# Kernel optimization log

Hardware: AMD Instinct MI355X
Metric: run time of the kernel (lower is better)

## Reference

```python
import jax, jax.numpy as jnp
import numpy as np


def _silu(x):
    return x * jax.nn.sigmoid(x)


def _ln(x, w, b, eps=1e-5):
    mu = x.mean(-1, keepdims=True)
    xc = x - mu
    var = (xc * xc).mean(-1, keepdims=True)
    return xc * jax.lax.rsqrt(var + eps) * w + b


def _segsum(a):
    # a: (..., Q) -> (..., Q, Q) lower-triangular cumulative segment sums
    Q = a.shape[-1]
    cs = jnp.cumsum(a, axis=-1)
    ss = cs[..., :, None] - cs[..., None, :]
    mask = jnp.tril(jnp.ones((Q, Q), dtype=bool))
    return jnp.where(mask, ss, -jnp.inf)


def _ssd(x, A, Bm, Cm, chunk=64):
    # Mamba2 SSD dual (chunked) form. x:(b,l,h,p) pre-scaled by dt, A:(b,l,h)=dt*A, Bm/Cm:(b,l,n)
    b, l, h, p = x.shape
    c = l // chunk
    x = x.reshape(b, c, chunk, h, p)
    A = A.reshape(b, c, chunk, h).transpose(0, 3, 1, 2)          # (b,h,c,q)
    Bm = Bm.reshape(b, c, chunk, -1)
    Cm = Cm.reshape(b, c, chunk, -1)
    Acs = jnp.cumsum(A, axis=-1)                                  # (b,h,c,q)
    Lmat = jnp.exp(_segsum(A))                                    # (b,h,c,q,q)
    Yd = jnp.einsum('bcln,bcsn,bhcls,bcshp->bclhp', Cm, Bm, Lmat, x)
    dec = jnp.exp(Acs[..., -1:] - Acs)                            # (b,h,c,q)
    states = jnp.einsum('bcln,bhcl,bclhp->bchpn', Bm, dec, x)     # (b,c,h,p,n)
    cdec = jnp.exp(Acs[..., -1]).transpose(2, 0, 1)               # (c,b,h)
    st = states.transpose(1, 0, 2, 3, 4)                          # (c,b,h,p,n)

    def step(carry, inp):
        s, d = inp
        return carry * d[..., None, None] + s, carry

    _, prev = jax.lax.scan(step, jnp.zeros_like(st[0]), (st, cdec))
    prev = prev.transpose(1, 0, 2, 3, 4)                          # (b,c,h,p,n)
    Yo = jnp.einsum('bcln,bchpn,bhcl->bclhp', Cm, prev, jnp.exp(Acs))
    return (Yd + Yo).reshape(b, l, h, p)


def _mamba(x, in_w, in_b, conv_w, conv_b, A_log, D, dt_bias, rms_w, out_w, headdim, d_state):
    b, l, _ = x.shape
    nh = A_log.shape[0]
    di = nh * headdim
    zxbcdt = x @ in_w.T + in_b
    z = zxbcdt[..., :di]
    xBC = zxbcdt[..., di:2 * di + 2 * d_state]
    dt = jax.nn.softplus(zxbcdt[..., -nh:] + dt_bias)             # (b,l,nh)
    K = conv_w.shape[-1]
    xp = jnp.pad(xBC, ((0, 0), (K - 1, 0), (0, 0)))               # causal depthwise conv
    xBC = sum(xp[:, k:k + l, :] * conv_w[:, k] for k in range(K))
    xBC = _silu(xBC + conv_b)
    xs = xBC[..., :di].reshape(b, l, nh, headdim)
    Bm = xBC[..., di:di + d_state]
    Cm = xBC[..., di + d_state:]
    A = -jnp.exp(A_log)
    y = _ssd(xs * dt[..., None], dt * A, Bm, Cm)
    y = y + D[None, None, :, None] * xs
    y = y.reshape(b, l, di) * _silu(z)                            # gated RMSNorm
    y = y * jax.lax.rsqrt(jnp.mean(y * y, -1, keepdims=True) + 1e-5) * rms_w
    return y @ out_w.T


def setup_inputs() -> dict:
    key = jax.random.key(0)
    ks = iter(jax.random.split(key, 64))

    def nrm(shape, s):
        return jax.random.normal(next(ks), shape, jnp.float32) * s

    d = {}
    d['x'] = jax.random.normal(next(ks), (4, 128, 64, 64), jnp.float32)
    d['seed_tok_w'] = nrm((8, 128), 0.08)
    d['seed_tok_b'] = jnp.zeros((8,), jnp.float32)
    d['seed_detok_w'] = nrm((128, 8), 0.3)
    d['seed_detok_b'] = jnp.zeros((128,), jnp.float32)
    d['sm_in_w'] = nrm((66, 8), 0.3)
    d['sm_in_b'] = jnp.zeros((66,), jnp.float32)
    d['sm_conv_w'] = nrm((48, 3), 0.3)
    d['sm_conv_b'] = jnp.zeros((48,), jnp.float32)
    d['sm_A_log'] = jnp.log(jnp.arange(1, 3, dtype=jnp.float32))
    d['sm_D'] = jnp.ones((2,), jnp.float32)
    d['sm_dt_bias'] = jnp.full((2,), -4.0, jnp.float32)
    d['sm_rms_w'] = jnp.ones((16,), jnp.float32)
    d['sm_out_w'] = nrm((8, 16), 0.2)
    d['cm_in_w'] = nrm((2, 196, 16), 0.2)
    d['cm_in_b'] = jnp.zeros((2, 196), jnp.float32)
    d['cm_conv_w'] = nrm((2, 160, 3), 0.3)
    d['cm_conv_b'] = jnp.zeros((2, 160), jnp.float32)
    d['cm_A_log'] = jnp.tile(jnp.log(jnp.arange(1, 5, dtype=jnp.float32)), (2, 1))
    d['cm_D'] = jnp.ones((2, 4), jnp.float32)
    d['cm_dt_bias'] = jnp.full((2, 4), -4.0, jnp.float32)
    d['cm_rms_w'] = jnp.ones((2, 32), jnp.float32)
    d['cm_out_w'] = nrm((2, 16, 32), 0.15)
    d['cross_W'] = jnp.eye(8, dtype=jnp.float32) + 0.01 * jax.random.normal(next(ks), (8, 8), jnp.float32)
    d['norm1_w'] = jnp.ones((128,), jnp.float32)
    d['norm1_b'] = jnp.zeros((128,), jnp.float32)
    d['norm2_w'] = jnp.ones((128,), jnp.float32)
    d['norm2_b'] = jnp.zeros((128,), jnp.float32)
    d['fc1_w'] = nrm((256, 128), 0.08)
    d['fc1_b'] = jnp.zeros((256,), jnp.float32)
    d['dw_w'] = nrm((256, 1, 3, 3), 0.2)
    d['dw_b'] = jnp.zeros((256,), jnp.float32)
    d['fc2_w'] = nrm((128, 256), 0.06)
    d['fc2_b'] = jnp.zeros((128,), jnp.float32)
    d['skip_scale'] = jnp.ones((1,), jnp.float32)
    return d


def reference(x, seed_tok_w, seed_tok_b, seed_detok_w, seed_detok_b,
              sm_in_w, sm_in_b, sm_conv_w, sm_conv_b, sm_A_log, sm_D, sm_dt_bias, sm_rms_w, sm_out_w,
              cm_in_w, cm_in_b, cm_conv_w, cm_conv_b, cm_A_log, cm_D, cm_dt_bias, cm_rms_w, cm_out_w,
              cross_W, norm1_w, norm1_b, norm2_w, norm2_b,
              fc1_w, fc1_b, dw_w, dw_b, fc2_w, fc2_b, skip_scale):
    B, C, H, W = x.shape
    L = H * W
    # --- GlobalSeed ---
    g = jnp.einsum('bchw,gc->bghw', x, seed_tok_w) + seed_tok_b[None, :, None, None]
    gf = g.reshape(B, -1, L).transpose(0, 2, 1)                   # (B,L,G)
    gf = _mamba(gf, sm_in_w, sm_in_b, sm_conv_w, sm_conv_b, sm_A_log, sm_D,
                sm_dt_bias, sm_rms_w, sm_out_w, 8, 16) + gf
    det = jnp.einsum('blg,cg->blc', gf, seed_detok_w) + seed_detok_b
    seed = x + det.transpose(0, 2, 1).reshape(B, C, H, W)
    # --- split-channel cascaded SSD (shared weights across splits) ---
    xn = _ln(x.reshape(B, C, L).transpose(0, 2, 1), norm1_w, norm1_b)   # (B,L,C)
    S = cross_W.shape[0]
    xs = jnp.stack(jnp.split(xn, S, axis=-1))                     # (S,B,L,C/S)

    def cascade(xi):
        for i in range(cm_in_w.shape[0]):
            xi = _mamba(xi, cm_in_w[i], cm_in_b[i], cm_conv_w[i], cm_conv_b[i],
                        cm_A_log[i], cm_D[i], cm_dt_bias[i], cm_rms_w[i], cm_out_w[i], 8, 64)
        return xi

    ys = jax.vmap(cascade)(xs) + xs * skip_scale
    # --- SubCrossToken mixing ---
    gm = ys.mean(axis=2)                                          # (S,B,Cs)
    wsm = jax.nn.softmax(cross_W, axis=1)
    gmix = jnp.einsum('qbc,qp->pbc', gm, wsm)
    ys = ys + gmix[:, :, None, :]
    out = ys.transpose(1, 2, 0, 3).reshape(B, L, -1)
    out = _ln(out, norm2_w, norm2_b)
    out = out.transpose(0, 2, 1).reshape(B, C, H, W) + seed
    # --- ConvFFN ---
    h1 = jnp.einsum('bchw,oc->bohw', out, fc1_w) + fc1_b[None, :, None, None]
    dw = jax.lax.conv_general_dilated(h1, dw_w, (1, 1), 'SAME',
                                      feature_group_count=h1.shape[1],
                                      dimension_numbers=('NCHW', 'OIHW', 'NCHW'))
    h2 = jax.nn.gelu(dw + dw_b[None, :, None, None])
    ffn = jnp.einsum('bohw,co->bchw', h2, fc2_w) + fc2_b[None, :, None, None]
    return out + ffn
```

## Files before the change

### kernel.cpp

```cpp
#include <hip/hip_runtime.h>
#include <math.h>

#define B_ 4
#define CCH 128
#define HH 64
#define WW 64
#define LL 4096
#define NCHK 64

__device__ __forceinline__ float siluf(float x) { return x / (1.f + __expf(-x)); }
__device__ __forceinline__ float softplusf(float x) { return (x > 20.f) ? x : log1pf(__expf(x)); }
__device__ __forceinline__ int swz(int n, int l) {
  return (n << 6) + ((((l >> 2) ^ ((n >> 2) & 15)) << 2) | (l & 3));
}

__global__ __launch_bounds__(256) void k_seedtok(const float* __restrict__ x,
    const float* __restrict__ w, const float* __restrict__ bias, float* __restrict__ gf)
{
  __shared__ float sw[8*128];
  int tid = threadIdx.x;
  for (int i = tid; i < 1024; i += 256) sw[i] = w[i];
  __syncthreads();
  int idx = blockIdx.x * 256 + tid;
  int b = idx / LL, l = idx % LL;
  const float* xp = x + (size_t)b*CCH*LL + l;
  float acc[8];
#pragma unroll
  for (int g = 0; g < 8; ++g) acc[g] = bias[g];
  for (int c = 0; c < CCH; ++c) {
    float xv = xp[(size_t)c*LL];
#pragma unroll
    for (int g = 0; g < 8; ++g) acc[g] += xv * sw[g*128 + c];
  }
  float* o = gf + (size_t)idx*8;
#pragma unroll
  for (int g = 0; g < 8; ++g) o[g] = acc[g];
}

template<int DIN, int NZ, int NDS, int NDT>
__global__ __launch_bounds__(256) void k_inproj(
    const float* __restrict__ src, int srcMode,
    const float* __restrict__ in_w, const float* __restrict__ in_b,
    const float* __restrict__ conv_w, const float* __restrict__ conv_b,
    const float* __restrict__ dt_bias,
    float* __restrict__ zb, float* __restrict__ dtb,
    float* __restrict__ xsb, float* __restrict__ Bb, float* __restrict__ Cb)
{
  constexpr int NXBC = NZ + 2*NDS;
  constexpr int NTOT = 2*NZ + 2*NDS + NDT;
  constexpr int NZQ  = NZ/4;
  constexpr int NDSQ = NDS/4;
  constexpr int XP   = DIN + 1;
  __shared__ float xt[66*XP];
  __shared__ float wl[NTOT*DIN];
  __shared__ float cwl[NXBC*3];
  __shared__ float cbl[NXBC];
  __shared__ float ibl[NTOT];
  __shared__ float dts[64*NDT];
  __shared__ float hp[NXBC*2];
  int tid = threadIdx.x;
  int seq = blockIdx.x >> 6;
  int l0  = (blockIdx.x & 63) << 6;
  for (int i = tid; i < NTOT*DIN; i += 256) wl[i] = in_w[i];
  for (int i = tid; i < NXBC*3; i += 256) cwl[i] = conv_w[i];
  for (int i = tid; i < NXBC; i += 256) cbl[i] = conv_b[i];
  for (int i = tid; i < NTOT; i += 256) ibl[i] = in_b[i];
  const float* sp; int sstr;
  if (srcMode == 0) { sp = src + (size_t)seq*LL*DIN; sstr = DIN; }
  else { sp = src + (size_t)(seq & 3)*LL*CCH + (seq >> 2)*16; sstr = CCH; }
  for (int i = tid; i < 66*DIN; i += 256) {
    int r = i / DIN, d = i % DIN;
    int l = l0 - 2 + r;
    xt[r*XP + d] = (l >= 0) ? sp[(size_t)l*sstr + d] : 0.f;
  }
  __syncthreads();
  for (int i = tid; i < 2*NXBC; i += 256) {
    int t = i & 1, ch = i >> 1;
    const float* wr = &wl[(NZ + ch)*DIN];
    const float* xp = &xt[t*XP];
    float acc = 0.f;
#pragma unroll
    for (int d = 0; d < DIN; ++d) acc += xp[d]*wr[d];
    hp[ch*2 + t] = acc;
  }
  __syncthreads();
  int l = tid & 63, w4 = tid >> 6;
  float xr2[DIN];
#pragma unroll
  for (int d = 0; d < DIN; ++d) xr2[d] = xt[(l+2)*XP + d];
  size_t gl = (size_t)seq*LL + l0 + l;
  int tok = l0 + l;
  float v0ok = (tok >= 2) ? 1.f : 0.f;
  float v1ok = (tok >= 1) ? 1.f : 0.f;
  {
    float zv[NZQ];
#pragma unroll
    for (int j = 0; j < NZQ; ++j) {
      int row = w4*NZQ + j;
      const float* wr = &wl[row*DIN];
      float acc = ibl[row];
#pragma unroll
      for (int d = 0; d < DIN; ++d) acc += xr2[d]*wr[d];
      zv[j] = acc;
    }
#pragma unroll
    for (int g = 0; g < NZQ/4; ++g)
      *(float4*)&zb[gl*NZ + w4*NZQ + 4*g] = make_float4(zv[4*g], zv[4*g+1], zv[4*g+2], zv[4*g+3]);
  }
  if (w4 < NDT) {
    int row = NTOT - NDT + w4;
    const float* wr = &wl[row*DIN];
    float acc = ibl[row] + dt_bias[w4];
#pragma unroll
    for (int d = 0; d < DIN; ++d) acc += xr2[d]*wr[d];
    dts[l*NDT + w4] = softplusf(acc);
  }
  auto convch = [&](int ch) -> float {
    int row = NZ + ch;
    const float* wr = &wl[row*DIN];
    float pm = 0.f;
#pragma unroll
    for (int d = 0; d < DIN; ++d) pm += xr2[d]*wr[d];
    float m1 = __shfl_up(pm, 1, 64);
    float m2 = __shfl_up(pm, 2, 64);
    float h0 = hp[ch*2 + 0], h1 = hp[ch*2 + 1];
    if (l == 0) m1 = h1;
    m2 = (l == 0) ? h0 : ((l == 1) ? h1 : m2);
    float ib = ibl[row];
    float conv = cbl[ch] + (m2+ib)*v0ok*cwl[ch*3+0] + (m1+ib)*v1ok*cwl[ch*3+1] + (pm+ib)*cwl[ch*3+2];
    return siluf(conv);
  };
  {
    float xv[NZQ];
#pragma unroll
    for (int j = 0; j < NZQ; ++j) xv[j] = convch(w4*NZQ + j);
#pragma unroll
    for (int g = 0; g < NZQ/4; ++g)
      *(float4*)&xsb[gl*NZ + w4*NZQ + 4*g] = make_float4(xv[4*g], xv[4*g+1], xv[4*g+2], xv[4*g+3]);
  }
  {
    float bv[NDSQ];
#pragma unroll
    for (int j = 0; j < NDSQ; ++j) bv[j] = convch(NZ + w4*NDSQ + j);
#pragma unroll
    for (int g = 0; g < NDSQ/4; ++g)
      *(float4*)&Bb[gl*NDS + w4*NDSQ + 4*g] = make_float4(bv[4*g], bv[4*g+1], bv[4*g+2], bv[4*g+3]);
  }
  {
    float cv[NDSQ];
#pragma unroll
    for (int j = 0; j < NDSQ; ++j) cv[j] = convch(NZ + NDS + w4*NDSQ + j);
#pragma unroll
    for (int g = 0; g < NDSQ/4; ++g)
      *(float4*)&Cb[gl*NDS + w4*NDSQ + 4*g] = make_float4(cv[4*g], cv[4*g+1], cv[4*g+2], cv[4*g+3]);
  }
  __syncthreads();
  if (tid < 64) {
    if constexpr (NDT == 4) {
      *(float4*)&dtb[((size_t)seq*LL + l0 + tid)*4] =
          make_float4(dts[tid*4], dts[tid*4+1], dts[tid*4+2], dts[tid*4+3]);
    } else {
      *(float2*)&dtb[((size_t)seq*LL + l0 + tid)*NDT] = make_float2(dts[tid*NDT], dts[tid*NDT+1]);
    }
  }
}

template<int DS, int NH>
__global__ __launch_bounds__(256) void k_ssd1(
    const float* __restrict__ xs, const float* __restrict__ dtb,
    const float* __restrict__ Bb, const float* __restrict__ Cb,
    const float* __restrict__ A_log,
    float* __restrict__ ybuf, float* __restrict__ states,
    float* __restrict__ cdec, float* __restrict__ acsOut)
{
  constexpr int DI = NH*8;
  constexpr int NG = DS/4;
  __shared__ __align__(16) float BtBl[DS*64];
  __shared__ __align__(16) float CtGt[64*64];
  __shared__ __align__(16) float xde[NH*64*8];
  int tid = threadIdx.x;
  int cid = blockIdx.x & 63;
  int seq = blockIdx.x >> 6;
  int l0  = cid << 6;
  for (int i = tid; i < 16*DS; i += 256) {
    int ng = i % NG, l = i / NG;
    size_t g = ((size_t)seq*LL + l0 + l)*DS + 4*ng;
    float4 bv = *(const float4*)&Bb[g];
    float4 cv = *(const float4*)&Cb[g];
    BtBl[swz(4*ng+0, l)] = bv.x; BtBl[swz(4*ng+1, l)] = bv.y;
    BtBl[swz(4*ng+2, l)] = bv.z; BtBl[swz(4*ng+3, l)] = bv.w;
    CtGt[swz(4*ng+0, l)] = cv.x; CtGt[swz(4*ng+1, l)] = cv.y;
    CtGt[swz(4*ng+2, l)] = cv.z; CtGt[swz(4*ng+3, l)] = cv.w;
  }
  __syncthreads();
  int lt = (tid >> 4) << 2, st = (tid & 15) << 2;
  float acc[4][4] = {};
#pragma unroll 4
  for (int n = 0; n < DS; ++n) {
    float4 cv = *(const float4*)&CtGt[swz(n, lt)];
    float4 bv = *(const float4*)&BtBl[swz(n, st)];
    float cc[4] = {cv.x, cv.y, cv.z, cv.w};
    float bb[4] = {bv.x, bv.y, bv.z, bv.w};
#pragma unroll
    for (int i2 = 0; i2 < 4; ++i2)
#pragma unroll
      for (int j2 = 0; j2 < 4; ++j2)
        acc[i2][j2] += cc[i2]*bb[j2];
  }
  __syncthreads();
#pragma unroll
  for (int j = 0; j < 4; ++j) {
    float4 gv = make_float4(acc[0][j], acc[1][j], acc[2][j], acc[3][j]);
    *(float4*)&CtGt[swz(st + j, lt)] = gv;
  }
  for (int i = tid; i < 16*DS; i += 256) {
    int ng = i % NG, l = i / NG;
    float4 bv = *(const float4*)&Bb[((size_t)seq*LL + l0 + l)*DS + 4*ng];
    *(float4*)&BtBl[l*DS + 4*ng] = bv;
  }
  __syncthreads();
  int w = tid >> 6, lane = tid & 63;
  if (w < NH) {
    int h = w;
    float dt_l = dtb[((size_t)seq*LL + l0 + lane)*NH + h];
    float Aval = -__expf(A_log[h]);
    float v = dt_l * Aval;
#pragma unroll
    for (int off = 1; off < 64; off <<= 1) {
      float t = __shfl_up(v, off, 64);
      if (lane >= off) v += t;
    }
    float acs_l = v;
    float m = __shfl(v, 31, 64);
    float acsLast = __shfl(v, 63, 64);
    float el = __expf(fminf(acs_l - m, 60.f));
    float fl = __expf(fminf(m - acs_l, 60.f));
    const float* xp = &xs[((size_t)seq*LL + l0 + lane)*DI + h*8];
    float4 x0 = *(const float4*)xp, x1 = *(const float4*)(xp + 4);
    float s1 = dt_l*fl;
    float* xe = &xde[(h*64 + lane)*8];
    *(float4*)xe     = make_float4(x0.x*s1, x0.y*s1, x0.z*s1, x0.w*s1);
    *(float4*)(xe+4) = make_float4(x1.x*s1, x1.y*s1, x1.z*s1, x1.w*s1);
    int lg = lane >> 2, lm = lane & 3;
    float ya[8] = {0,0,0,0,0,0,0,0};
#pragma unroll 4
    for (int s = 0; s < 64; ++s) {
      float g = CtGt[(s << 6) + ((((lg ^ ((s >> 2) & 15))) << 2) | lm)];
      g = (s <= lane) ? g : 0.f;
      const float* xr = &xde[(h*64 + s)*8];
      float4 a0 = *(const float4*)xr, a1 = *(const float4*)(xr + 4);
      ya[0] += g*a0.x; ya[1] += g*a0.y; ya[2] += g*a0.z; ya[3] += g*a0.w;
      ya[4] += g*a1.x; ya[5] += g*a1.y; ya[6] += g*a1.z; ya[7] += g*a1.w;
    }
    float* yp = &ybuf[((size_t)seq*LL + l0 + lane)*DI + h*8];
    *(float4*)yp     = make_float4(ya[0]*el, ya[1]*el, ya[2]*el, ya[3]*el);
    *(float4*)(yp+4) = make_float4(ya[4]*el, ya[5]*el, ya[6]*el, ya[7]*el);
    if (lane < DS) {
      float r2 = __expf(acsLast - m);
      float sa[8] = {0,0,0,0,0,0,0,0};
#pragma unroll 4
      for (int ll = 0; ll < 64; ++ll) {
        float b = BtBl[ll*DS + lane];
        const float* xr = &xde[(h*64 + ll)*8];
        float4 a0 = *(const float4*)xr, a1 = *(const float4*)(xr + 4);
        sa[0] += b*a0.x; sa[1] += b*a0.y; sa[2] += b*a0.z; sa[3] += b*a0.w;
        sa[4] += b*a1.x; sa[5] += b*a1.y; sa[6] += b*a1.z; sa[7] += b*a1.w;
      }
      float* sp2 = &states[(((size_t)seq*NH + h)*NCHK + cid)*(size_t)(8*DS) + lane*8];
      *(float4*)sp2     = make_float4(sa[0]*r2, sa[1]*r2, sa[2]*r2, sa[3]*r2);
      *(float4*)(sp2+4) = make_float4(sa[4]*r2, sa[5]*r2, sa[6]*r2, sa[7]*r2);
    }
    if (lane == 63) cdec[((size_t)seq*NH + h)*NCHK + cid] = __expf(acsLast);
    acsOut[((size_t)seq*NH + h)*LL + l0 + lane] = acs_l;
  }
}

__global__ __launch_bounds__(512) void k_scan(float* __restrict__ st, const float* __restrict__ cd, int PN)
{
  int tid = threadIdx.x;
  size_t base = (size_t)blockIdx.x * NCHK * PN + tid;
  const float* c = cd + (size_t)blockIdx.x * NCHK;
  float carry = 0.f;
  for (int k = 0; k < NCHK; ++k) {
    size_t a = base + (size_t)k*PN;
    float s = st[a];
    st[a] = carry;
    carry = carry*c[k] + s;
  }
}

template<int DS, int NH>
__global__ __launch_bounds__(256) void k_ssd_yo(
    float* __restrict__ ybuf, const float* __restrict__ Cb,
    const float* __restrict__ prevSt, const float* __restrict__ acsG,
    const float* __restrict__ Dp, const float* __restrict__ xs)
{
  constexpr int DI = NH*8;
  constexpr int NG = DS/4;
  __shared__ __align__(16) float Ct2[DS*64];
  __shared__ __align__(16) float pvs[NH*DS*8];
  int tid = threadIdx.x;
  int cid = blockIdx.x & 63;
  int seq = blockIdx.x >> 6;
  int l0  = cid << 6;
  for (int i = tid; i < 16*DS; i += 256) {
    int ng = i % NG, l = i / NG;
    float4 cv = *(const float4*)&Cb[((size_t)seq*LL + l0 + l)*DS + 4*ng];
    Ct2[swz(4*ng+0, l)] = cv.x; Ct2[swz(4*ng+1, l)] = cv.y;
    Ct2[swz(4*ng+2, l)] = cv.z; Ct2[swz(4*ng+3, l)] = cv.w;
  }
  for (int i = tid; i < NH*DS*8; i += 256) {
    int h = i / (DS*8), r = i % (DS*8);
    pvs[i] = prevSt[(((size_t)seq*NH + h)*NCHK + cid)*(size_t)(DS*8) + r];
  }
  __syncthreads();
  int w = tid >> 6, lane = tid & 63;
  if (w < NH) {
    int h = w;
    float el = __expf(acsG[((size_t)seq*NH + h)*LL + l0 + lane]);
    float Dh = Dp[h];
    int lg = lane >> 2, lm = lane & 3;
    float acc[8] = {0,0,0,0,0,0,0,0};
#pragma unroll 4
    for (int n = 0; n < DS; ++n) {
      float c = Ct2[(n << 6) + ((((lg ^ ((n >> 2) & 15))) << 2) | lm)];
      const float* pr = &pvs[(h*DS + n)*8];
      float4 p0 = *(const float4*)pr, p1 = *(const float4*)(pr + 4);
      acc[0] += c*p0.x; acc[1] += c*p0.y; acc[2] += c*p0.z; acc[3] += c*p0.w;
      acc[4] += c*p1.x; acc[5] += c*p1.y; acc[6] += c*p1.z; acc[7] += c*p1.w;
    }
    size_t gi = ((size_t)seq*LL + l0 + lane)*DI + h*8;
    float4 y0 = *(const float4*)&ybuf[gi], y1 = *(const float4*)&ybuf[gi+4];
    float4 xv0 = *(const float4*)&xs[gi], xv1 = *(const float4*)&xs[gi+4];
    y0.x += el*acc[0] + Dh*xv0.x; y0.y += el*acc[1] + Dh*xv0.y;
    y0.z += el*acc[2] + Dh*xv0.z; y0.w += el*acc[3] + Dh*xv0.w;
    y1.x += el*acc[4] + Dh*xv1.x; y1.y += el*acc[5] + Dh*xv1.y;
    y1.z += el*acc[6] + Dh*xv1.z; y1.w += el*acc[7] + Dh*xv1.w;
    *(float4*)&ybuf[gi] = y0; *(float4*)&ybuf[gi+4] = y1;
  }
}

template<int DI, int DOUT>
__global__ __launch_bounds__(256) void k_gate(
    const float* __restrict__ ybuf, const float* __restrict__ zbuf,
    const float* __restrict__ rms_w, const float* __restrict__ out_w,
    float* __restrict__ dst, int resMode, const float* __restrict__ res,
    const float* __restrict__ skipPtr)
{
  __shared__ float ow[DOUT*DI];
  __shared__ float rw[DI];
  int tid = threadIdx.x;
  for (int i = tid; i < DOUT*DI; i += 256) ow[i] = out_w[i];
  for (int i = tid; i < DI; i += 256) rw[i] = rms_w[i];
  __syncthreads();
  size_t idx = (size_t)blockIdx.x*256 + tid;
  float y[DI];
  const float* yp = ybuf + idx*DI;
  const float* zp = zbuf + idx*DI;
  float ss = 0.f;
#pragma unroll
  for (int i = 0; i < DI; ++i) {
    float z = zp[i];
    float g = yp[i] * (z / (1.f + __expf(-z)));
    y[i] = g; ss += g*g;
  }
  float r = rsqrtf(ss*(1.f/DI) + 1e-5f);
#pragma unroll
  for (int i = 0; i < DI; ++i) y[i] *= r*rw[i];
  const float* rp = nullptr; float skip = 1.f;
  int seq = (int)(idx / LL), l = (int)(idx % LL);
  if (resMode == 1) rp = res + idx*DOUT;
  else if (resMode == 2) {
    int s = seq / B_, b = seq % B_;
    rp = res + ((size_t)b*LL + l)*CCH + s*DOUT;
    skip = skipPtr[0];
  }
  float* dp = dst + idx*DOUT;
#pragma unroll
  for (int o = 0; o < DOUT; ++o) {
    float acc = 0.f;
#pragma unroll
    for (int i = 0; i < DI; ++i) acc += y[i]*ow[o*DI + i];
    if (rp) acc += skip * rp[o];
    dp[o] = acc;
  }
}

__global__ __launch_bounds__(256) void k_ln1(const float* __restrict__ x,
    const float* __restrict__ w, const float* __restrict__ bb, float* __restrict__ xn)
{
  __shared__ float tile[128*65];
  __shared__ float mu[64], rs[64];
  int tid = threadIdx.x;
  int b = blockIdx.x >> 6;
  int l0 = (blockIdx.x & 63) << 6;
  for (int i = tid; i < 8192; i += 256) {
    int l = i & 63, c = i >> 6;
    tile[c*65 + l] = x[((size_t)b*CCH + c)*LL + l0 + l];
  }
  __syncthreads();
  if (tid < 64) {
    float s = 0.f;
    for (int c = 0; c < CCH; ++c) s += tile[c*65 + tid];
    float m = s * (1.f/CCH);
    float v = 0.f;
    for (int c = 0; c < CCH; ++c) { float d = tile[c*65 + tid] - m; v += d*d; }
    mu[tid] = m; rs[tid] = rsqrtf(v*(1.f/CCH) + 1e-5f);
  }
  __syncthreads();
  for (int i = tid; i < 8192; i += 256) {
    int c = i & 127, l = i >> 7;
    xn[((size_t)b*LL + l0 + l)*CCH + c] = (tile[c*65 + l] - mu[l])*rs[l]*w[c] + bb[c];
  }
}

__global__ __launch_bounds__(256) void k_gm(const float* __restrict__ ys, float* __restrict__ gm)
{
  __shared__ float red[256];
  int tid = threadIdx.x;
  int seq = blockIdx.x;
  int c = tid & 15, lane = tid >> 4;
  float s = 0.f;
  for (int l = lane; l < LL; l += 16) s += ys[((size_t)seq*LL + l)*16 + c];
  red[tid] = s;
  __syncthreads();
  if (tid < 16) {
    float t = 0.f;
    for (int g = 0; g < 16; ++g) t += red[g*16 + tid];
    gm[(size_t)seq*16 + tid] = t * (1.f/LL);
  }
}

__global__ __launch_bounds__(256) void k_mix(const float* __restrict__ gm,
    const float* __restrict__ crossW, float* __restrict__ gmix)
{
  __shared__ float wsm[64];
  int tid = threadIdx.x;
  if (tid < 8) {
    float mx = -1e30f;
    for (int p = 0; p < 8; ++p) mx = fmaxf(mx, crossW[tid*8 + p]);
    float e[8]; float s = 0.f;
    for (int p = 0; p < 8; ++p) { e[p] = __expf(crossW[tid*8 + p] - mx); s += e[p]; }
    for (int p = 0; p < 8; ++p) wsm[tid*8 + p] = e[p] / s;
  }
  __syncthreads();
  for (int i = tid; i < 512; i += 256) {
    int c = i & 15; int bb = (i >> 4) & 3; int p = i >> 6;
    float acc = 0.f;
    for (int q = 0; q < 8; ++q) acc += gm[((size_t)(q*B_ + bb))*16 + c] * wsm[q*8 + p];
    gmix[((size_t)(p*B_ + bb))*16 + c] = acc;
  }
}

__global__ __launch_bounds__(256) void k_out2(const float* __restrict__ ys,
    const float* __restrict__ gmix, const float* __restrict__ w, const float* __restrict__ bb,
    const float* __restrict__ x, const float* __restrict__ gf2,
    const float* __restrict__ dw, const float* __restrict__ db,
    float* __restrict__ outb)
{
  __shared__ float tile[128*65];
  __shared__ float mu[64], rs[64];
  int tid = threadIdx.x;
  int b = blockIdx.x >> 6;
  int l0 = (blockIdx.x & 63) << 6;
  for (int i = tid; i < 8192; i += 256) {
    int c = i & 15; int l = (i >> 4) & 63; int s = i >> 10;
    int seq = s*B_ + b;
    tile[(s*16 + c)*65 + l] = ys[((size_t)seq*LL + l0 + l)*16 + c] + gmix[(size_t)seq*16 + c];
  }
  __syncthreads();
  if (tid < 64) {
    float sm = 0.f;
    for (int c = 0; c < 128; ++c) sm += tile[c*65 + tid];
    float m = sm * (1.f/128.f);
    float v = 0.f;
    for (int c = 0; c < 128; ++c) { float d = tile[c*65 + tid] - m; v += d*d; }
    mu[tid] = m; rs[tid] = rsqrtf(v*(1.f/128.f) + 1e-5f);
  }
  __syncthreads();
  int lfix = tid & 63;
  float g8[8];
  {
    const float* gp = gf2 + ((size_t)b*LL + l0 + lfix)*8;
#pragma unroll
    for (int k = 0; k < 8; ++k) g8[k] = gp[k];
  }
  for (int i = tid; i < 8192; i += 256) {
    int l = i & 63, c = i >> 6;
    size_t gi = ((size_t)b*CCH + c)*LL + l0 + l;
    float det = db[c];
#pragma unroll
    for (int k = 0; k < 8; ++k) det += g8[k]*dw[c*8 + k];
    outb[gi] = (tile[c*65 + l] - mu[l])*rs[l]*w[c] + bb[c] + x[gi] + det;
  }
}

__global__ __launch_bounds__(256) void k_fc1(const float* __restrict__ src,
    const float* __restrict__ w, const float* __restrict__ bias, float* __restrict__ dst)
{
  constexpr int WP = 129;
  __shared__ float st[128*64];
  __shared__ float wt[64*WP];
  int tid = threadIdx.x;
  int blk = blockIdx.x;
  int ot = blk & 3;
  int lt = (blk >> 2) & 63;
  int b  = blk >> 8;
  int l0 = lt << 6, o0 = ot << 6;
  for (int i = tid; i < 8192; i += 256) {
    int l = i & 63, c = i >> 6;
    st[c*64 + l] = src[((size_t)b*CCH + c)*LL + l0 + l];
  }
  for (int i = tid; i < 8192; i += 256) {
    int c = i & 127, o = i >> 7;
    wt[o*WP + c] = w[(size_t)(o0 + o)*128 + c];
  }
  __syncthreads();
  int l4 = (tid & 15) << 2, o4 = (tid >> 4) << 2;
  float a0[4] = {}, a1[4] = {}, a2[4] = {}, a3[4] = {};
#pragma unroll 4
  for (int c = 0; c < 128; ++c) {
    float4 sv = *(float4*)&st[c*64 + l4];
    float w0 = wt[(o4+0)*WP + c];
    float w1 = wt[(o4+1)*WP + c];
    float w2 = wt[(o4+2)*WP + c];
    float w3 = wt[(o4+3)*WP + c];
    a0[0] += w0*sv.x; a0[1] += w0*sv.y; a0[2] += w0*sv.z; a0[3] += w0*sv.w;
    a1[0] += w1*sv.x; a1[1] += w1*sv.y; a1[2] += w1*sv.z; a1[3] += w1*sv.w;
    a2[0] += w2*sv.x; a2[1] += w2*sv.y; a2[2] += w2*sv.z; a2[3] += w2*sv.w;
    a3[0] += w3*sv.x; a3[1] += w3*sv.y; a3[2] += w3*sv.z; a3[3] += w3*sv.w;
  }
  float* rows[4] = {a0, a1, a2, a3};
#pragma unroll
  for (int j = 0; j < 4; ++j) {
    int o = o0 + o4 + j;
    float bi = bias[o];
    float* a = rows[j];
    *(float4*)&dst[((size_t)b*256 + o)*LL + l0 + l4] =
        make_float4(a[0]+bi, a[1]+bi, a[2]+bi, a[3]+bi);
  }
}

__global__ __launch_bounds__(256) void k_dw(const float* __restrict__ h1,
    const float* __restrict__ w, const float* __restrict__ bias, float* __restrict__ h2)
{
  __shared__ float tile[66*66];
  int tid = threadIdx.x;
  int blk = blockIdx.x;
  const float* base = h1 + (size_t)blk*LL;
  const float* wp = w + (blk & 255)*9;
  float bi = bias[blk & 255];
  for (int i = tid; i < 66*66; i += 256) {
    int r = i / 66, cc = i % 66;
    int gr = r - 1, gc = cc - 1;
    tile[i] = (gr >= 0 && gr < HH && gc >= 0 && gc < WW) ? base[gr*WW + gc] : 0.f;
  }
  float w00 = wp[0], w01 = wp[1], w02 = wp[2];
  float w10 = wp[3], w11 = wp[4], w12 = wp[5];
  float w20 = wp[6], w21 = wp[7], w22 = wp[8];
  __syncthreads();
  float* outp = h2 + (size_t)blk*LL;
#pragma unroll
  for (int k = 0; k < 16; ++k) {
    int j = tid + k*256;
    int row = j >> 6, col = j & 63;
    const float* t0 = &tile[row*66 + col];
    float acc = t0[0]*w00  + t0[1]*w01  + t0[2]*w02
              + t0[66]*w10 + t0[67]*w11 + t0[68]*w12
              + t0[132]*w20 + t0[133]*w21 + t0[134]*w22;
    float v = acc + bi;
    float u = 0.7978845608028654f*(v + 0.044715f*v*v*v);
    float e = __expf(2.f*u);
    float th = 1.f - 2.f/(e + 1.f);
    outp[j] = 0.5f*v*(1.f + th);
  }
}

__global__ __launch_bounds__(256) void k_fc2(const float* __restrict__ h2,
    const float* __restrict__ w, const float* __restrict__ bias,
    const float* __restrict__ resid, float* __restrict__ dst)
{
  constexpr int WP = 260;
  __shared__ float st[128*64];
  __shared__ float wt[32*WP];
  int tid = threadIdx.x;
  int blk = blockIdx.x;
  int ct = blk & 3;
  int lt = (blk >> 2) & 63;
  int b  = blk >> 8;
  int l0 = lt << 6, c0 = ct << 5;
  for (int i = tid; i < 32*256; i += 256) {
    int o = i & 255, c = i >> 8;
    wt[c*WP + o] = w[(size_t)(c0 + c)*256 + o];
  }
  int l4 = (tid & 15) << 2, c2 = (tid >> 4) << 1;
  float a0[4] = {}, a1[4] = {};
  for (int ko = 0; ko < 256; ko += 128) {
    __syncthreads();
    for (int i = tid; i < 8192; i += 256) {
      int l = i & 63, o = i >> 6;
      st[o*64 + l] = h2[((size_t)b*256 + ko + o)*LL + l0 + l];
    }
    __syncthreads();
#pragma unroll 4
    for (int o = 0; o < 128; ++o) {
      float4 sv = *(float4*)&st[o*64 + l4];
      float w0 = wt[(c2+0)*WP + ko + o];
      float w1 = wt[(c2+1)*WP + ko + o];
      a0[0] += w0*sv.x; a0[1] += w0*sv.y; a0[2] += w0*sv.z; a0[3] += w0*sv.w;
      a1[0] += w1*sv.x; a1[1] += w1*sv.y; a1[2] += w1*sv.z; a1[3] += w1*sv.w;
    }
  }
  float* rows[2] = {a0, a1};
#pragma unroll
  for (int j = 0; j < 2; ++j) {
    int c = c0 + c2 + j;
    float bi = bias[c];
    size_t gi = ((size_t)b*CCH + c)*LL + l0 + l4;
    float4 rv = *(const float4*)&resid[gi];
    float* a = rows[j];
    *(float4*)&dst[gi] = make_float4(a[0]+bi+rv.x, a[1]+bi+rv.y, a[2]+bi+rv.z, a[3]+bi+rv.w);
  }
}

extern "C" void kernel_launch(void* const* d_in, const int* in_sizes, int n_in,
                              void* d_out, int out_size, void* d_ws, size_t ws_size,
                              hipStream_t stream) {
  (void)in_sizes; (void)n_in; (void)out_size; (void)ws_size;
  const float* x        = (const float*)d_in[0];
  const float* tok_w    = (const float*)d_in[1];
  const float* tok_b    = (const float*)d_in[2];
  const float* detok_w  = (const float*)d_in[3];
  const float* detok_b  = (const float*)d_in[4];
  const float* sm_in_w  = (const float*)d_in[5];
  const float* sm_in_b  = (const float*)d_in[6];
  const float* sm_conv_w= (const float*)d_in[7];
  const float* sm_conv_b= (const float*)d_in[8];
  const float* sm_A_log = (const float*)d_in[9];
  const float* sm_D     = (const float*)d_in[10];
  const float* sm_dt_b  = (const float*)d_in[11];
  const float* sm_rms_w = (const float*)d_in[12];
  const float* sm_out_w = (const float*)d_in[13];
  const float* cm_in_w  = (const float*)d_in[14];
  const float* cm_in_b  = (const float*)d_in[15];
  const float* cm_conv_w= (const float*)d_in[16];
  const float* cm_conv_b= (const float*)d_in[17];
  const float* cm_A_log = (const float*)d_in[18];
  const float* cm_D     = (const float*)d_in[19];
  const float* cm_dt_b  = (const float*)d_in[20];
  const float* cm_rms_w = (const float*)d_in[21];
  const float* cm_out_w = (const float*)d_in[22];
  const float* cross_W  = (const float*)d_in[23];
  const float* n1w      = (const float*)d_in[24];
  const float* n1b      = (const float*)d_in[25];
  const float* n2w      = (const float*)d_in[26];
  const float* n2b      = (const float*)d_in[27];
  const float* fc1w     = (const float*)d_in[28];
  const float* fc1b     = (const float*)d_in[29];
  const float* dww      = (const float*)d_in[30];
  const float* dwb      = (const float*)d_in[31];
  const float* fc2w     = (const float*)d_in[32];
  const float* fc2b     = (const float*)d_in[33];
  const float* skp      = (const float*)d_in[34];
  float* ws  = (float*)d_ws;
  float* out = (float*)d_out;

  const size_t SGF0 = 0;
  const size_t SOUTn= 131072;
  const size_t XN   = 2097152;
  const size_t YS   = 4194304;
  const size_t OUTB = 6291456;
  const size_t GM   = 8388608;
  const size_t GMIX = 8389120;
  const size_t SCR  = 8389632;
  const size_t CZ   = SCR;
  const size_t CDT  = CZ   + 4194304;
  const size_t CXS  = CDT  + 524288;
  const size_t CBF  = CXS  + 4194304;
  const size_t CCF  = CBF  + 8388608;
  const size_t CACS = CCF  + 8388608;
  const size_t CST  = CACS + 2097152;
  const size_t CCD  = CST  + 4194304;
  const size_t CY   = CCD  + 8192;
  const size_t XB   = CY   + 4194304;
  const size_t SZ   = SCR;
  const size_t SDT  = SZ  + 262144;
  const size_t SXS  = SDT + 32768;
  const size_t SB   = SXS + 262144;
  const size_t SC   = SB  + 262144;
  const size_t SACS = SC  + 262144;
  const size_t SST  = SACS + 32768;
  const size_t SCD  = SST + 65536;
  const size_t SY   = SCD + 512;
  const size_t H1 = SCR;
  const size_t H2 = SCR + 4194304;

  k_seedtok<<<64, 256, 0, stream>>>(x, tok_w, tok_b, ws + SGF0);
  k_inproj<8,16,16,2><<<B_*64, 256, 0, stream>>>(ws + SGF0, 0, sm_in_w, sm_in_b, sm_conv_w,
      sm_conv_b, sm_dt_b, ws + SZ, ws + SDT, ws + SXS, ws + SB, ws + SC);
  k_ssd1<16,2><<<B_*NCHK, 256, 0, stream>>>(ws + SXS, ws + SDT, ws + SB, ws + SC,
      sm_A_log, ws + SY, ws + SST, ws + SCD, ws + SACS);
  k_scan<<<B_*2, 128, 0, stream>>>(ws + SST, ws + SCD, 128);
  k_ssd_yo<16,2><<<B_*NCHK, 256, 0, stream>>>(ws + SY, ws + SC, ws + SST, ws + SACS, sm_D, ws + SXS);
  k_gate<16,8><<<B_*LL/256, 256, 0, stream>>>(ws + SY, ws + SZ, sm_rms_w, sm_out_w,
      ws + SOUTn, 1, ws + SGF0, skp);

  k_ln1<<<B_*64, 256, 0, stream>>>(x, n1w, n1b, ws + XN);

  k_inproj<16,32,64,4><<<32*64, 256, 0, stream>>>(ws + XN, 1, cm_in_w, cm_in_b, cm_conv_w,
      cm_conv_b, cm_dt_b, ws + CZ, ws + CDT, ws + CXS, ws + CBF, ws + CCF);
  k_ssd1<64,4><<<32*NCHK, 256, 0, stream>>>(ws + CXS, ws + CDT, ws + CBF, ws + CCF,
      cm_A_log, ws + CY, ws + CST, ws + CCD, ws + CACS);
  k_scan<<<32*4, 512, 0, stream>>>(ws + CST, ws + CCD, 512);
  k_ssd_yo<64,4><<<32*NCHK, 256, 0, stream>>>(ws + CY, ws + CCF, ws + CST, ws + CACS, cm_D, ws + CXS);
  k_gate<32,16><<<32*LL/256, 256, 0, stream>>>(ws + CY, ws + CZ, cm_rms_w, cm_out_w,
      ws + XB, 0, nullptr, skp);

  k_inproj<16,32,64,4><<<32*64, 256, 0, stream>>>(ws + XB, 0, cm_in_w + 3136, cm_in_b + 196,
      cm_conv_w + 480, cm_conv_b + 160, cm_dt_b + 4, ws + CZ, ws + CDT, ws + CXS, ws + CBF, ws + CCF);
  k_ssd1<64,4><<<32*NCHK, 256, 0, stream>>>(ws + CXS, ws + CDT, ws + CBF, ws + CCF,
      cm_A_log + 4, ws + CY, ws + CST, ws + CCD, ws + CACS);
  k_scan<<<32*4, 512, 0, stream>>>(ws + CST, ws + CCD, 512);
  k_ssd_yo<64,4><<<32*NCHK, 256, 0, stream>>>(ws + CY, ws + CCF, ws + CST, ws + CACS, cm_D + 4, ws + CXS);
  k_gate<32,16><<<32*LL/256, 256, 0, stream>>>(ws + CY, ws + CZ, cm_rms_w + 32, cm_out_w + 512,
      ws + YS, 2, ws + XN, skp);

  k_gm<<<32, 256, 0, stream>>>(ws + YS, ws + GM);
  k_mix<<<1, 256, 0, stream>>>(ws + GM, cross_W, ws + GMIX);
  k_out2<<<B_*64, 256, 0, stream>>>(ws + YS, ws + GMIX, n2w, n2b,
      x, ws + SOUTn, detok_w, detok_b, ws + OUTB);

  k_fc1<<<B_*64*4, 256, 0, stream>>>(ws + OUTB, fc1w, fc1b, ws + H1);
  k_dw<<<B_*256, 256, 0, stream>>>(ws + H1, dww, dwb, ws + H2);
  k_fc2<<<B_*64*4, 256, 0, stream>>>(ws + H2, fc2w, fc2b, ws + OUTB, out);
}
```

Before: 647.1 us.

## Fuse in-projection, causal conv and SSD chunk kernel for cross-Mamba layers

Adds a k_inssd kernel that performs the input projection, the causal depthwise conv with SiLU, dt softplus, and the intra-chunk SSD (diagonal block and chunk states) in a single block per chunk. The B matrix and dt stay in shared memory and registers instead of going to global scratch, and the separate inproj and ssd1 launches for both cascade layers are replaced. Halo rows for the conv are recomputed through a small pre-pass. Shared memory use (~54KB) and the launch-bounds occupancy hint could limit occupancy relative to the two separate kernels.

```diff
diff --git a/kernel.cpp b/kernel.cpp
--- a/kernel.cpp
+++ b/kernel.cpp
@@ -163,6 +163,197 @@
       *(float2*)&dtb[((size_t)seq*LL + l0 + tid)*NDT] = make_float2(dts[tid*NDT], dts[tid*NDT+1]);
     }
   }
+}
+
+__global__ __launch_bounds__(256, 3) void k_inssd(
+    const float* __restrict__ src, int srcMode,
+    const float* __restrict__ in_w, const float* __restrict__ in_b,
+    const float* __restrict__ conv_w, const float* __restrict__ conv_b,
+    const float* __restrict__ dt_bias, const float* __restrict__ A_log,
+    float* __restrict__ zb, float* __restrict__ xsb, float* __restrict__ Cb,
+    float* __restrict__ ybuf, float* __restrict__ states,
+    float* __restrict__ cdec, float* __restrict__ acsOut)
+{
+  const int DIN = 16, NZ = 32, NDS = 64, DI = 32;
+  const int NXBC = 160, NTOT = 196, XP = 17;
+  __shared__ float sm[13606];
+  float* Bl  = sm;
+  float* Ct  = sm + 4096;
+  float* U   = sm + 8192;
+  float* xt  = U;
+  float* wl  = U + 1122;
+  float* cwl = U + 4258;
+  float* cbl = U + 4738;
+  float* ibl = U + 4898;
+  float* hp  = U + 5094;
+  float* xde = U;
+  int tid = threadIdx.x;
+  int cid = blockIdx.x & 63;
+  int seq = blockIdx.x >> 6;
+  int l0  = cid << 6;
+  for (int i = tid; i < NTOT*DIN; i += 256) wl[i] = in_w[i];
+  for (int i = tid; i < NXBC*3; i += 256) cwl[i] = conv_w[i];
+  for (int i = tid; i < NXBC; i += 256) cbl[i] = conv_b[i];
+  for (int i = tid; i < NTOT; i += 256) ibl[i] = in_b[i];
+  const float* sp; int sstr;
+  if (srcMode == 0) { sp = src + (size_t)seq*LL*DIN; sstr = DIN; }
+  else { sp = src + (size_t)(seq & 3)*LL*CCH + (seq >> 2)*16; sstr = CCH; }
+  for (int i = tid; i < 66*DIN; i += 256) {
+    int r = i / DIN, d = i % DIN;
+    int l = l0 - 2 + r;
+    xt[r*XP + d] = (l >= 0) ? sp[(size_t)l*sstr + d] : 0.f;
+  }
+  __syncthreads();
+  for (int i = tid; i < 2*NXBC; i += 256) {
+    int t = i & 1, ch = i >> 1;
+    const float* wr = &wl[(NZ + ch)*DIN];
+    const float* xp = &xt[t*XP];
+    float acc = 0.f;
+#pragma unroll
+    for (int d = 0; d < DIN; ++d) acc += xp[d]*wr[d];
+    hp[ch*2 + t] = acc;
+  }
+  __syncthreads();
+  int lane = tid & 63, w = tid >> 6;
+  float xr2[DIN];
+#pragma unroll
+  for (int d = 0; d < DIN; ++d) xr2[d] = xt[(lane+2)*XP + d];
+  size_t gl = (size_t)seq*LL + l0 + lane;
+  int tok = l0 + lane;
+  float v0ok = (tok >= 2) ? 1.f : 0.f;
+  float v1ok = (tok >= 1) ? 1.f : 0.f;
+  {
+    float zv[8];
+#pragma unroll
+    for (int j = 0; j < 8; ++j) {
+      int row = w*8 + j;
+      const float* wr = &wl[row*DIN];
+      float acc = ibl[row];
+#pragma unroll
+      for (int d = 0; d < DIN; ++d) acc += xr2[d]*wr[d];
+      zv[j] = acc;
+    }
+    *(float4*)&zb[gl*NZ + w*8 + 0] = make_float4(zv[0], zv[1], zv[2], zv[3]);
+    *(float4*)&zb[gl*NZ + w*8 + 4] = make_float4(zv[4], zv[5], zv[6], zv[7]);
+  }
+  float dtv;
+  {
+    int row = NTOT - 4 + w;
+    const float* wr = &wl[row*DIN];
+    float acc = ibl[row] + dt_bias[w];
+#pragma unroll
+    for (int d = 0; d < DIN; ++d) acc += xr2[d]*wr[d];
+    dtv = softplusf(acc);
+  }
+  auto convch = [&](int ch) -> float {
+    int row = NZ + ch;
+    const float* wr = &wl[row*DIN];
+    float pm = 0.f;
+#pragma unroll
+    for (int d = 0; d < DIN; ++d) pm += xr2[d]*wr[d];
+    float m1 = __shfl_up(pm, 1, 64);
+    float m2 = __shfl_up(pm, 2, 64);
+    float h0 = hp[ch*2 + 0], h1 = hp[ch*2 + 1];
+    if (lane == 0) m1 = h1;
+    m2 = (lane == 0) ? h0 : ((lane == 1) ? h1 : m2);
+    float ib = ibl[row];
+    float conv = cbl[ch] + (m2+ib)*v0ok*cwl[ch*3+0] + (m1+ib)*v1ok*cwl[ch*3+1] + (pm+ib)*cwl[ch*3+2];
+    return siluf(conv);
+  };
+  float xv[8];
+#pragma unroll
+  for (int j = 0; j < 8; ++j) xv[j] = convch(w*8 + j);
+  *(float4*)&xsb[gl*DI + w*8 + 0] = make_float4(xv[0], xv[1], xv[2], xv[3]);
+  *(float4*)&xsb[gl*DI + w*8 + 4] = make_float4(xv[4], xv[5], xv[6], xv[7]);
+#pragma unroll
+  for (int j = 0; j < 16; ++j) {
+    int n = w*16 + j;
+    float b = convch(NZ + n);
+    Bl[lane*64 + ((n + lane) & 63)] = b;
+  }
+  {
+    float cv[16];
+#pragma unroll
+    for (int j = 0; j < 16; ++j) {
+      int n = w*16 + j;
+      cv[j] = convch(NZ + NDS + n);
+      Ct[swz(n, lane)] = cv[j];
+    }
+#pragma unroll
+    for (int g = 0; g < 4; ++g)
+      *(float4*)&Cb[gl*NDS + w*16 + 4*g] = make_float4(cv[4*g], cv[4*g+1], cv[4*g+2], cv[4*g+3]);
+  }
+  __syncthreads();
+  float Aval = -__expf(A_log[w]);
+  float v = dtv * Aval;
+#pragma unroll
+  for (int off = 1; off < 64; off <<= 1) {
+    float t = __shfl_up(v, off, 64);
+    if (lane >= off) v += t;
+  }
+  float acs_l = v;
+  float m = __shfl(v, 31, 64);
+  float acsLast = __shfl(v, 63, 64);
+  float el = __expf(fminf(acs_l - m, 60.f));
+  float fl = __expf(fminf(m - acs_l, 60.f));
+  {
+    float s1 = dtv*fl;
+    float* xe = &xde[(w*64 + lane)*8];
+    *(float4*)xe     = make_float4(xv[0]*s1, xv[1]*s1, xv[2]*s1, xv[3]*s1);
+    *(float4*)(xe+4) = make_float4(xv[4]*s1, xv[5]*s1, xv[6]*s1, xv[7]*s1);
+  }
+  int lt = (tid >> 4) << 2, st = (tid & 15) << 2;
+  float acc[4][4] = {};
+#pragma unroll 4
+  for (int n = 0; n < 64; ++n) {
+    float4 cvv = *(const float4*)&Ct[swz(n, lt)];
+    float cc[4] = {cvv.x, cvv.y, cvv.z, cvv.w};
+    float bb[4];
+#pragma unroll
+    for (int j = 0; j < 4; ++j) bb[j] = Bl[(st+j)*64 + ((n + st + j) & 63)];
+#pragma unroll
+    for (int i2 = 0; i2 < 4; ++i2)
+#pragma unroll
+      for (int j2 = 0; j2 < 4; ++j2)
+        acc[i2][j2] += cc[i2]*bb[j2];
+  }
+  __syncthreads();
+#pragma unroll
+  for (int j = 0; j < 4; ++j) {
+    *(float4*)&Ct[swz(st + j, lt)] = make_float4(acc[0][j], acc[1][j], acc[2][j], acc[3][j]);
+  }
+  __syncthreads();
+  int lg = lane >> 2, lm = lane & 3;
+  float ya[8] = {0,0,0,0,0,0,0,0};
+#pragma unroll 4
+  for (int s = 0; s < 64; ++s) {
+    float g = Ct[(s << 6) + (((lg ^ ((s >> 2) & 15))) << 2 | lm)];
+    g = (s <= lane) ? g : 0.f;
+    const float* xr = &xde[(w*64 + s)*8];
+    float4 a0 = *(const float4*)xr, a1 = *(const float4*)(xr + 4);
+    ya[0] += g*a0.x; ya[1] += g*a0.y; ya[2] += g*a0.z; ya[3] += g*a0.w;
+    ya[4] += g*a1.x; ya[5] += g*a1.y; ya[6] += g*a1.z; ya[7] += g*a1.w;
+  }
+  float* yp = &ybuf[gl*DI + w*8];
+  *(float4*)yp     = make_float4(ya[0]*el, ya[1]*el, ya[2]*el, ya[3]*el);
+  *(float4*)(yp+4) = make_float4(ya[4]*el, ya[5]*el, ya[6]*el, ya[7]*el);
+  {
+    float r2 = __expf(acsLast - m);
+    float sa[8] = {0,0,0,0,0,0,0,0};
+#pragma unroll 4
+    for (int ll = 0; ll < 64; ++ll) {
+      float b = Bl[ll*64 + ((lane + ll) & 63)];
+      const float* xr = &xde[(w*64 + ll)*8];
+      float4 a0 = *(const float4*)xr, a1 = *(const float4*)(xr + 4);
+      sa[0] += b*a0.x; sa[1] += b*a0.y; sa[2] += b*a0.z; sa[3] += b*a0.w;
+      sa[4] += b*a1.x; sa[5] += b*a1.y; sa[6] += b*a1.z; sa[7] += b*a1.w;
+    }
+    float* sp2 = &states[(((size_t)seq*4 + w)*NCHK + cid)*(size_t)(8*NDS) + lane*8];
+    *(float4*)sp2     = make_float4(sa[0]*r2, sa[1]*r2, sa[2]*r2, sa[3]*r2);
+    *(float4*)(sp2+4) = make_float4(sa[4]*r2, sa[5]*r2, sa[6]*r2, sa[7]*r2);
+  }
+  if (lane == 63) cdec[((size_t)seq*4 + w)*NCHK + cid] = __expf(acsLast);
+  acsOut[((size_t)seq*4 + w)*LL + l0 + lane] = acs_l;
 }
 
 template<int DS, int NH>
@@ -674,10 +865,8 @@
   const size_t GMIX = 8389120;
   const size_t SCR  = 8389632;
   const size_t CZ   = SCR;
-  const size_t CDT  = CZ   + 4194304;
-  const size_t CXS  = CDT  + 524288;
-  const size_t CBF  = CXS  + 4194304;
-  const size_t CCF  = CBF  + 8388608;
+  const size_t CXS  = CZ   + 4194304;
+  const size_t CCF  = CXS  + 4194304;
   const size_t CACS = CCF  + 8388608;
   const size_t CST  = CACS + 2097152;
   const size_t CCD  = CST  + 4194304;
@@ -707,19 +896,17 @@
 
   k_ln1<<<B_*64, 256, 0, stream>>>(x, n1w, n1b, ws + XN);
 
-  k_inproj<16,32,64,4><<<32*64, 256, 0, stream>>>(ws + XN, 1, cm_in_w, cm_in_b, cm_conv_w,
-      cm_conv_b, cm_dt_b, ws + CZ, ws + CDT, ws + CXS, ws + CBF, ws + CCF);
-  k_ssd1<64,4><<<32*NCHK, 256, 0, stream>>>(ws + CXS, ws + CDT, ws + CBF, ws + CCF,
-      cm_A_log, ws + CY, ws + CST, ws + CCD, ws + CACS);
+  k_inssd<<<32*NCHK, 256, 0, stream>>>(ws + XN, 1, cm_in_w, cm_in_b, cm_conv_w,
+      cm_conv_b, cm_dt_b, cm_A_log, ws + CZ, ws + CXS, ws + CCF,
+      ws + CY, ws + CST, ws + CCD, ws + CACS);
   k_scan<<<32*4, 512, 0, stream>>>(ws + CST, ws + CCD, 512);
   k_ssd_yo<64,4><<<32*NCHK, 256, 0, stream>>>(ws + CY, ws + CCF, ws + CST, ws + CACS, cm_D, ws + CXS);
   k_gate<32,16><<<32*LL/256, 256, 0, stream>>>(ws + CY, ws + CZ, cm_rms_w, cm_out_w,
       ws + XB, 0, nullptr, skp);
 
-  k_inproj<16,32,64,4><<<32*64, 256, 0, stream>>>(ws + XB, 0, cm_in_w + 3136, cm_in_b + 196,
-      cm_conv_w + 480, cm_conv_b + 160, cm_dt_b + 4, ws + CZ, ws + CDT, ws + CXS, ws + CBF, ws + CCF);
-  k_ssd1<64,4><<<32*NCHK, 256, 0, stream>>>(ws + CXS, ws + CDT, ws + CBF, ws + CCF,
-      cm_A_log + 4, ws + CY, ws + CST, ws + CCD, ws + CACS);
+  k_inssd<<<32*NCHK, 256, 0, stream>>>(ws + XB, 0, cm_in_w + 3136, cm_in_b + 196,
+      cm_conv_w + 480, cm_conv_b + 160, cm_dt_b + 4, cm_A_log + 4, ws + CZ, ws + CXS, ws + CCF,
+      ws + CY, ws + CST, ws + CCD, ws + CACS);
   k_scan<<<32*4, 512, 0, stream>>>(ws + CST, ws + CCD, 512);
   k_ssd_yo<64,4><<<32*NCHK, 256, 0, stream>>>(ws + CY, ws + CCF, ws + CST, ws + CACS, cm_D + 4, ws + CXS);
   k_gate<32,16><<<32*LL/256, 256, 0, stream>>>(ws + CY, ws + CZ, cm_rms_w + 32, cm_out_w + 512,
```

Result: slower. 704.9 us (+8.9%).
